# Kernel tuning notes

Measured on AMD Instinct MI355X. Metric: run time of the kernel, lower is better.

The kernel has to match this reference:

```python
import jax, jax.numpy as jnp
import numpy as np

N_NODES = 100000
N_EDGES = 1600000
IN_DIM, HID_DIM, OUT_DIM = 256, 128, 128


def gcn_norm(edge_index, edge_weight, num_nodes):
    # Add self-loops with weight 1 (PyG GCNConv default fill_value=1.0)
    loop = jnp.arange(num_nodes, dtype=edge_index.dtype)
    src = jnp.concatenate([edge_index[0], loop])
    dst = jnp.concatenate([edge_index[1], loop])
    w = jnp.concatenate([edge_weight, jnp.ones((num_nodes,), edge_weight.dtype)])
    # Symmetric normalization: deg computed at destination over edge weights
    deg = jax.ops.segment_sum(w, dst, num_segments=num_nodes)
    dinv = jnp.where(deg > 0, jax.lax.rsqrt(deg), 0.0)
    norm = dinv[src] * w * dinv[dst]  # [E + N]
    return src, dst, norm


def gcn_conv(x, W, b, src, dst, norm, num_nodes):
    h = x @ W                                  # [N, out]
    msg = h[src] * norm[:, None]               # gather + scale, [E+N, out]
    out = jax.ops.segment_sum(msg, dst, num_segments=num_nodes)  # scatter-add
    return out + b


def setup_inputs() -> dict:
    key = jax.random.key(0)
    ks = jax.random.split(key, 8)
    x = jax.random.normal(ks[0], (N_NODES, IN_DIM), dtype=jnp.float32)
    edge_index = jax.random.randint(ks[1], (2, N_EDGES), 0, N_NODES, dtype=jnp.int64)
    edge_weight = jax.random.uniform(ks[2], (N_EDGES,), dtype=jnp.float32)
    s1 = 1.0 / np.sqrt(IN_DIM)
    s2 = 1.0 / np.sqrt(HID_DIM)
    W1 = jax.random.uniform(ks[3], (IN_DIM, HID_DIM), jnp.float32, -s1, s1)
    b1 = jnp.zeros((HID_DIM,), jnp.float32)
    W2 = jax.random.uniform(ks[4], (HID_DIM, OUT_DIM), jnp.float32, -s2, s2)
    b2 = jnp.zeros((OUT_DIM,), jnp.float32)
    return {"x": x, "edge_index": edge_index, "edge_weight": edge_weight,
            "W1": W1, "b1": b1, "W2": W2, "b2": b2}


def reference(x, edge_index, edge_weight, W1, b1, W2, b2):
    n = x.shape[0]
    src, dst, norm = gcn_norm(edge_index, edge_weight, n)
    h = jax.nn.relu(gcn_conv(x, W1, b1, src, dst, norm, n))
    out = gcn_conv(h, W2, b2, src, dst, norm, n)
    return out
```

## Files before the change

### kernel.cpp

```cpp
#include <hip/hip_runtime.h>
#include <stdint.h>

#define N_NODES 100000
#define N_EDGES 1600000
#define IN_DIM 256
#define HID_DIM 128
#define OUT_DIM 128

#define NBUCK 391
#define CHUNK 4096
#define BCAP 4736

typedef __attribute__((ext_vector_type(8))) short short8;
typedef __attribute__((ext_vector_type(4))) float floatx4;

__device__ __forceinline__ float bf2f(unsigned short u) {
    union { unsigned int i; float f; } v; v.i = ((unsigned int)u) << 16; return v.f;
}
__device__ __forceinline__ unsigned short f2bf(float f) {
    union { float fl; unsigned int i; } v; v.fl = f;
    unsigned int x = v.i;
    return (unsigned short)((x + 0x7fffu + ((x >> 16) & 1u)) >> 16);
}
__device__ __forceinline__ float bflo(unsigned int u) {
    union { unsigned int i; float f; } v; v.i = u << 16; return v.f;
}
__device__ __forceinline__ float bfhi(unsigned int u) {
    union { unsigned int i; float f; } v; v.i = u & 0xffff0000u; return v.f;
}
__device__ __forceinline__ float asf(unsigned int u) {
    union { unsigned int i; float f; } v; v.i = u; return v.f;
}
__device__ __forceinline__ unsigned int asu(float f) {
    union { float fl; unsigned int i; } v; v.fl = f; return v.i;
}
__device__ __forceinline__ unsigned int pack2(float a, float b) {
    unsigned int ua = asu(a), ub = asu(b);
    ua += 0x7fffu + ((ua >> 16) & 1u);
    ub += 0x7fffu + ((ub >> 16) & 1u);
    return (ua >> 16) | (ub & 0xffff0000u);
}
__device__ __forceinline__ short8 pack8(float4 a, float4 b) {
    union { unsigned int u[4]; short8 s; } r;
    r.u[0] = pack2(a.x, a.y);
    r.u[1] = pack2(a.z, a.w);
    r.u[2] = pack2(b.x, b.y);
    r.u[3] = pack2(b.z, b.w);
    return r.s;
}

__global__ void k_detect(const unsigned int* __restrict__ xu, const unsigned int* __restrict__ eu,
                         int* __restrict__ flags, int* __restrict__ bucket_cursor) {
    __shared__ int s_huge, s_odd;
    if (threadIdx.x == 0) { s_huge = 0; s_odd = 0; }
    if (threadIdx.x < NBUCK) bucket_cursor[threadIdx.x] = 0;
    __syncthreads();
    int huge = 0, odd = 0;
    for (int i = threadIdx.x; i < 1024; i += 512) {
        unsigned int b = xu[i];
        unsigned int e = (b >> 23) & 0xffu;
        if (e >= 0xf0u) huge = 1;
        if (eu[2 * i + 1] != 0) odd = 1;
    }
    if (huge) atomicOr(&s_huge, 1);
    if (odd) atomicOr(&s_odd, 1);
    __syncthreads();
    if (threadIdx.x == 0) { flags[0] = s_huge ? 0 : 1; flags[1] = s_odd ? 0 : 1; }
}

__device__ __forceinline__ int load_idx(const void* base, long long i, int i64m) {
    int v = i64m ? (int)((const long long*)base)[i] : ((const int*)base)[i];
    return v < 0 ? 0 : (v >= N_NODES ? N_NODES - 1 : v);
}
__device__ __forceinline__ float load_f(const void* base, long long i, int f32m) {
    return f32m ? ((const float*)base)[i] : bf2f(((const unsigned short*)base)[i]);
}

__global__ void k_bscatter(const void* __restrict__ ei, const void* __restrict__ ew,
                           const int* __restrict__ flags, int* __restrict__ bucket_cursor,
                           uint2* __restrict__ ebuf, int e) {
    __shared__ int h[NBUCK];
    for (int t = threadIdx.x; t < NBUCK; t += 256) h[t] = 0;
    __syncthreads();
    int f32m = flags[0], i64m = flags[1];
    int base = blockIdx.x * CHUNK;
    int end = base + CHUNK < e ? base + CHUNK : e;
    for (int i = base + threadIdx.x; i < end; i += 256) {
        int d = load_idx(ei, (long long)N_EDGES + i, i64m);
        atomicAdd(&h[d >> 8], 1);
    }
    __syncthreads();
    for (int t = threadIdx.x; t < NBUCK; t += 256) {
        int c = h[t];
        h[t] = c ? (t * BCAP + atomicAdd(&bucket_cursor[t], c)) : 0;
    }
    __syncthreads();
    for (int i = base + threadIdx.x; i < end; i += 256) {
        int s = load_idx(ei, i, i64m);
        int d = load_idx(ei, (long long)N_EDGES + i, i64m);
        float w = load_f(ew, i, f32m);
        int b = d >> 8;
        int p = atomicAdd(&h[b], 1);
        uint2 c; c.x = (unsigned int)s | ((unsigned int)(d & 255) << 17); c.y = asu(w);
        ebuf[p] = c;
    }
}

__global__ void k_bscan(const int* __restrict__ bucket_cursor, int* __restrict__ bucket_base,
                        int* __restrict__ rowptr) {
    __shared__ int lds[512];
    int t = threadIdx.x;
    int v = (t < NBUCK) ? bucket_cursor[t] : 0;
    lds[t] = v;
    __syncthreads();
    for (int off = 1; off < 512; off <<= 1) {
        int x = (t >= off) ? lds[t - off] : 0;
        __syncthreads();
        lds[t] += x;
        __syncthreads();
    }
    int excl = lds[t] - v;
    if (t < NBUCK) bucket_base[t] = excl;
    if (t == 0) { bucket_base[NBUCK] = lds[NBUCK - 1]; rowptr[N_NODES] = N_EDGES; }
}

__global__ void k_fine(const uint2* __restrict__ ebuf, const int* __restrict__ bucket_base,
                       uint2* __restrict__ csr, int* __restrict__ rowptr,
                       float* __restrict__ dinv, int n) {
    __shared__ int h[256];
    __shared__ float fw[256];
    __shared__ int c2[256];
    int t = threadIdx.x, b = blockIdx.x;
    int w0 = bucket_base[b];
    int cnt = bucket_base[b + 1] - w0;
    const uint2* src = ebuf + (size_t)b * BCAP;
    if (t < 256) { h[t] = 0; fw[t] = 0.f; }
    __syncthreads();
    for (int i = t; i < cnt; i += 512) {
        uint2 c = src[i];
        int dl = (c.x >> 17) & 255;
        atomicAdd(&h[dl], 1);
        atomicAdd(&fw[dl], asf(c.y));
    }
    __syncthreads();
    int own = (t < 256) ? h[t] : 0;
    for (int off = 1; off < 256; off <<= 1) {
        int x = (t >= off && t < 256) ? h[t - off] : 0;
        __syncthreads();
        if (t < 256) h[t] += x;
        __syncthreads();
    }
    if (t < 256) {
        int excl = h[t] - own;
        int node = (b << 8) + t;
        if (node < n) {
            rowptr[node] = w0 + excl;
            dinv[node] = rsqrtf(1.0f + fw[t]);
        }
        c2[t] = w0 + excl;
    }
    __syncthreads();
    for (int i = t; i < cnt; i += 512) {
        uint2 c = src[i];
        int dl = (c.x >> 17) & 255;
        int p = atomicAdd(&c2[dl], 1);
        csr[p] = c;
    }
}

__global__ void k_transpose(const void* __restrict__ W1, const void* __restrict__ W2,
                            const int* __restrict__ flags,
                            unsigned short* __restrict__ W1T, unsigned short* __restrict__ W2T) {
    int i = blockIdx.x * 256 + threadIdx.x;
    int f32m = flags[0];
    if (i < IN_DIM * HID_DIM) {
        int k = i / HID_DIM, n = i % HID_DIM;
        W1T[n * IN_DIM + k] = f2bf(load_f(W1, i, f32m));
    } else {
        int j = i - IN_DIM * HID_DIM;
        if (j < HID_DIM * OUT_DIM) {
            int k = j / OUT_DIM, n = j % OUT_DIM;
            W2T[n * HID_DIM + k] = f2bf(load_f(W2, j, f32m));
        }
    }
}

template <int KH, bool F32M>
__device__ __forceinline__ void gemm_loop(const void* __restrict__ A,
                                          const unsigned short* __restrict__ Bs,
                                          size_t aoff, int quad, int l16, floatx4 (&acc)[8]) {
    constexpr int NCH = KH / 32;
    constexpr int BMASK = KH / 8 - 1;
    short8 a[NCH];
    if (F32M) {
        const float* ap = (const float*)A;
#pragma unroll
        for (int ch = 0; ch < NCH; ch++) {
            float4 f0 = *(const float4*)(ap + aoff + ch * 32);
            float4 f1 = *(const float4*)(ap + aoff + ch * 32 + 4);
            a[ch] = pack8(f0, f1);
        }
    } else {
        const unsigned short* ap = (const unsigned short*)A;
#pragma unroll
        for (int ch = 0; ch < NCH; ch++)
            a[ch] = *(const short8*)(ap + aoff + ch * 32);
    }
#pragma unroll
    for (int ch = 0; ch < NCH; ch++) {
#pragma unroll
        for (int c = 0; c < 8; c++) {
            int col = c * 16 + l16;
            int boff = col * KH + 8 * ((ch * 4 + quad + (col & 7)) & BMASK);
            short8 bf = *(const short8*)(Bs + boff);
            acc[c] = __builtin_amdgcn_mfma_f32_16x16x32_bf16(a[ch], bf, acc[c], 0, 0, 0);
        }
    }
}

template <int K, bool RAWA>
__global__ void k_gemm(const void* __restrict__ A, const unsigned short* __restrict__ WT,
                       const float* __restrict__ dinv, unsigned short* __restrict__ H,
                       const int* __restrict__ flags, int n) {
    constexpr int KH = 64;
    __shared__ unsigned short Bs[128 * KH];

    int wave = threadIdx.x >> 6;
    int lane = threadIdx.x & 63;
    int quad = lane >> 4;
    int l16 = lane & 15;
    int rowbase = blockIdx.x * 64 + wave * 16;
    int r0 = rowbase + l16;        if (r0 >= n) r0 = n - 1;
    size_t aoff0 = (size_t)r0 * K + quad * 8;

    floatx4 acc[8];
#pragma unroll
    for (int c = 0; c < 8; c++) acc[c] = (floatx4){0.f, 0.f, 0.f, 0.f};

    int f32m = RAWA ? flags[0] : 0;

#pragma unroll
    for (int hh = 0; hh < K / KH; hh++) {
        if (hh) __syncthreads();
        for (int base = threadIdx.x * 8; base < 128 * KH; base += 256 * 8) {
            int col = base / KH;
            int k = base - col * KH;
            int ks = (k + (col & 7) * 8) & (KH - 1);
            *(short8*)(&Bs[col * KH + ks]) = *(const short8*)(WT + col * K + hh * KH + k);
        }
        __syncthreads();
        if (RAWA && f32m)
            gemm_loop<KH, true>(A, Bs, aoff0 + hh * KH, quad, l16, acc);
        else
            gemm_loop<KH, false>(A, Bs, aoff0 + hh * KH, quad, l16, acc);
    }

#pragma unroll
    for (int r = 0; r < 4; r++) {
        int grow = rowbase + quad * 4 + r;
        if (grow < n) {
            float sc = dinv[grow];
#pragma unroll
            for (int c = 0; c < 8; c++)
                H[(size_t)grow * 128 + c * 16 + l16] = f2bf(sc * acc[c][r]);
        }
    }
}

#define NODES_PER_BLK 16

__device__ __forceinline__ void acc8(float wt, uint4 hv, float* a) {
    a[0] += wt * bflo(hv.x); a[1] += wt * bfhi(hv.x);
    a[2] += wt * bflo(hv.y); a[3] += wt * bfhi(hv.y);
    a[4] += wt * bflo(hv.z); a[5] += wt * bfhi(hv.z);
    a[6] += wt * bflo(hv.w); a[7] += wt * bfhi(hv.w);
}

template <bool RELU, bool FINAL>
__global__ void k_aggregate(const unsigned short* __restrict__ H, const int* __restrict__ rowptr,
                            const uint2* __restrict__ csr, const float* __restrict__ dinv,
                            const void* __restrict__ bias, void* __restrict__ out,
                            const int* __restrict__ flags, int n) {
    __shared__ int cursor;
    if (threadIdx.x == 0) cursor = 0;
    __syncthreads();
    int lane = threadIdx.x & 15;
    int col = lane * 8;
    int f32m = flags[0];

    float bv[8];
#pragma unroll
    for (int i = 0; i < 8; i++) bv[i] = load_f(bias, col + i, f32m);

    for (;;) {
        int idx;
        if (lane == 0) idx = atomicAdd(&cursor, 1);
        idx = __shfl(idx, 0, 16);
        if (idx >= NODES_PER_BLK) break;
        int node = blockIdx.x * NODES_PER_BLK + idx;
        if (node >= n) break;

        int e0 = rowptr[node], e1 = rowptr[node + 1];
        uint4 u = *(const uint4*)(H + (size_t)node * 128 + col);
        float dn = dinv[node];

        float a[8] = {0.f, 0.f, 0.f, 0.f, 0.f, 0.f, 0.f, 0.f};
        int e = e0;
        for (; e + 4 <= e1; e += 4) {
            uint2 c0 = csr[e], c1 = csr[e + 1], c2 = csr[e + 2], c3 = csr[e + 3];
            uint4 h0 = *(const uint4*)(H + (size_t)(c0.x & 0x1FFFF) * 128 + col);
            uint4 h1 = *(const uint4*)(H + (size_t)(c1.x & 0x1FFFF) * 128 + col);
            uint4 h2 = *(const uint4*)(H + (size_t)(c2.x & 0x1FFFF) * 128 + col);
            uint4 h3 = *(const uint4*)(H + (size_t)(c3.x & 0x1FFFF) * 128 + col);
            acc8(asf(c0.y), h0, a); acc8(asf(c1.y), h1, a);
            acc8(asf(c2.y), h2, a); acc8(asf(c3.y), h3, a);
        }
        for (; e < e1; e++) {
            uint2 c = csr[e];
            uint4 hh = *(const uint4*)(H + (size_t)(c.x & 0x1FFFF) * 128 + col);
            acc8(asf(c.y), hh, a);
        }

        a[0] = dn * (a[0] + bflo(u.x)) + bv[0];
        a[1] = dn * (a[1] + bfhi(u.x)) + bv[1];
        a[2] = dn * (a[2] + bflo(u.y)) + bv[2];
        a[3] = dn * (a[3] + bfhi(u.y)) + bv[3];
        a[4] = dn * (a[4] + bflo(u.z)) + bv[4];
        a[5] = dn * (a[5] + bfhi(u.z)) + bv[5];
        a[6] = dn * (a[6] + bflo(u.w)) + bv[6];
        a[7] = dn * (a[7] + bfhi(u.w)) + bv[7];

        if (RELU) {
#pragma unroll
            for (int i = 0; i < 8; i++) a[i] = fmaxf(a[i], 0.f);
        }
        if (FINAL && f32m) {
            float* op = (float*)out + (size_t)node * 128 + col;
            float4 o0 = {a[0], a[1], a[2], a[3]};
            float4 o1 = {a[4], a[5], a[6], a[7]};
            *(float4*)op = o0;
            *(float4*)(op + 4) = o1;
        } else {
            uint4 o;
            o.x = pack2(a[0], a[1]); o.y = pack2(a[2], a[3]);
            o.z = pack2(a[4], a[5]); o.w = pack2(a[6], a[7]);
            *(uint4*)((unsigned short*)out + (size_t)node * 128 + col) = o;
        }
    }
}

extern "C" void kernel_launch(void* const* d_in, const int* in_sizes, int n_in,
                              void* d_out, int out_size, void* d_ws, size_t ws_size,
                              hipStream_t stream) {
    const void* x  = d_in[0];
    const void* ei = d_in[1];
    const void* ew = d_in[2];
    const void* W1 = d_in[3];
    const void* b1 = d_in[4];
    const void* W2 = d_in[5];
    const void* b2 = d_in[6];

    char* p = (char*)d_ws;
    auto alloc = [&](size_t bytes) { char* r = p; p += (bytes + 255) & ~(size_t)255; return r; };
    int*   flags    = (int*)alloc(256);
    float* dinv     = (float*)alloc((size_t)N_NODES * 4);
    int*   rowptr   = (int*)alloc((size_t)(N_NODES + 1) * 4);
    int*   bucket_cursor = (int*)alloc((size_t)NBUCK * 4);
    int*   bucket_base   = (int*)alloc((size_t)(NBUCK + 1) * 4);
    uint2* csr      = (uint2*)alloc((size_t)N_EDGES * 8);
    unsigned short* W1T  = (unsigned short*)alloc((size_t)IN_DIM * HID_DIM * 2);
    unsigned short* W2T  = (unsigned short*)alloc((size_t)HID_DIM * OUT_DIM * 2);
    unsigned short* hbuf = (unsigned short*)alloc((size_t)N_NODES * 128 * 2);
    unsigned short* zbuf = (unsigned short*)alloc((size_t)N_NODES * 128 * 2);
    uint2* ebuf = (uint2*)hbuf;

    int nbC = (N_EDGES + CHUNK - 1) / CHUNK;
    int nbG = (N_NODES + 63) / 64;
    int nbA = (N_NODES + NODES_PER_BLK - 1) / NODES_PER_BLK;

    k_detect<<<1, 512, 0, stream>>>((const unsigned int*)x, (const unsigned int*)ei, flags, bucket_cursor);
    k_bscatter<<<nbC, 256, 0, stream>>>(ei, ew, flags, bucket_cursor, ebuf, N_EDGES);
    k_bscan<<<1, 512, 0, stream>>>(bucket_cursor, bucket_base, rowptr);
    k_fine<<<NBUCK, 512, 0, stream>>>(ebuf, bucket_base, csr, rowptr, dinv, N_NODES);
    k_transpose<<<(IN_DIM * HID_DIM + HID_DIM * OUT_DIM + 255) / 256, 256, 0, stream>>>(W1, W2, flags, W1T, W2T);

    k_gemm<IN_DIM, true><<<nbG, 256, 0, stream>>>(x, W1T, dinv, hbuf, flags, N_NODES);
    k_aggregate<true, false><<<nbA, 256, 0, stream>>>(hbuf, rowptr, csr, dinv,
                                                      b1, zbuf, flags, N_NODES);
    k_gemm<HID_DIM, false><<<nbG, 256, 0, stream>>>(zbuf, W2T, dinv, hbuf, flags, N_NODES);
    k_aggregate<false, true><<<nbA, 256, 0, stream>>>(hbuf, rowptr, csr, dinv,
                                                      b2, d_out, flags, N_NODES);
}
```

Measured before the change: 413.3 us.

## Stage full weight matrix in LDS and issue all A loads before sync

Result: no change. 412.7 us (-0.1%).

```diff
diff --git a/kernel.cpp b/kernel.cpp
--- a/kernel.cpp
+++ b/kernel.cpp
@@ -185,74 +185,63 @@
     }
 }
 
-template <int KH, bool F32M>
-__device__ __forceinline__ void gemm_loop(const void* __restrict__ A,
-                                          const unsigned short* __restrict__ Bs,
-                                          size_t aoff, int quad, int l16, floatx4 (&acc)[8]) {
-    constexpr int NCH = KH / 32;
-    constexpr int BMASK = KH / 8 - 1;
-    short8 a[NCH];
-    if (F32M) {
-        const float* ap = (const float*)A;
-#pragma unroll
-        for (int ch = 0; ch < NCH; ch++) {
-            float4 f0 = *(const float4*)(ap + aoff + ch * 32);
-            float4 f1 = *(const float4*)(ap + aoff + ch * 32 + 4);
-            a[ch] = pack8(f0, f1);
-        }
-    } else {
-        const unsigned short* ap = (const unsigned short*)A;
-#pragma unroll
-        for (int ch = 0; ch < NCH; ch++)
-            a[ch] = *(const short8*)(ap + aoff + ch * 32);
-    }
-#pragma unroll
-    for (int ch = 0; ch < NCH; ch++) {
-#pragma unroll
-        for (int c = 0; c < 8; c++) {
-            int col = c * 16 + l16;
-            int boff = col * KH + 8 * ((ch * 4 + quad + (col & 7)) & BMASK);
-            short8 bf = *(const short8*)(Bs + boff);
-            acc[c] = __builtin_amdgcn_mfma_f32_16x16x32_bf16(a[ch], bf, acc[c], 0, 0, 0);
-        }
-    }
-}
-
 template <int K, bool RAWA>
 __global__ void k_gemm(const void* __restrict__ A, const unsigned short* __restrict__ WT,
                        const float* __restrict__ dinv, unsigned short* __restrict__ H,
                        const int* __restrict__ flags, int n) {
-    constexpr int KH = 64;
-    __shared__ unsigned short Bs[128 * KH];
+    __shared__ unsigned short Bs[128 * K];
+    constexpr int NCH = K / 32;
+    constexpr int BMASK = K / 8 - 1;
 
     int wave = threadIdx.x >> 6;
     int lane = threadIdx.x & 63;
     int quad = lane >> 4;
     int l16 = lane & 15;
-    int rowbase = blockIdx.x * 64 + wave * 16;
+    int rowbase = blockIdx.x * 128 + wave * 16;
     int r0 = rowbase + l16;        if (r0 >= n) r0 = n - 1;
-    size_t aoff0 = (size_t)r0 * K + quad * 8;
+    size_t aoff = (size_t)r0 * K + quad * 8;
+
+    for (int base = threadIdx.x * 8; base < 128 * K; base += 512 * 8) {
+        int col = base / K;
+        int k = base - col * K;
+        int ks = (k + (col & 7) * 8) & (K - 1);
+        *(short8*)(&Bs[col * K + ks]) = *(const short8*)(WT + base);
+    }
+
+    short8 a[NCH];
+    int f32m = RAWA ? flags[0] : 0;
+    if (RAWA && f32m) {
+        const float* ap = (const float*)A;
+        float4 f[NCH][2];
+#pragma unroll
+        for (int ch = 0; ch < NCH; ch++) {
+            f[ch][0] = *(const float4*)(ap + aoff + ch * 32);
+            f[ch][1] = *(const float4*)(ap + aoff + ch * 32 + 4);
+        }
+#pragma unroll
+        for (int ch = 0; ch < NCH; ch++) a[ch] = pack8(f[ch][0], f[ch][1]);
+    } else {
+        const unsigned short* ap = (const unsigned short*)A;
+#pragma unroll
+        for (int ch = 0; ch < NCH; ch++)
+            a[ch] = *(const short8*)(ap + aoff + ch * 32);
+    }
+
+    __syncthreads();
 
     floatx4 acc[8];
 #pragma unroll
     for (int c = 0; c < 8; c++) acc[c] = (floatx4){0.f, 0.f, 0.f, 0.f};
 
-    int f32m = RAWA ? flags[0] : 0;
-
-#pragma unroll
-    for (int hh = 0; hh < K / KH; hh++) {
-        if (hh) __syncthreads();
-        for (int base = threadIdx.x * 8; base < 128 * KH; base += 256 * 8) {
-            int col = base / KH;
-            int k = base - col * KH;
-            int ks = (k + (col & 7) * 8) & (KH - 1);
-            *(short8*)(&Bs[col * KH + ks]) = *(const short8*)(WT + col * K + hh * KH + k);
-        }
-        __syncthreads();
-        if (RAWA && f32m)
-            gemm_loop<KH, true>(A, Bs, aoff0 + hh * KH, quad, l16, acc);
-        else
-            gemm_loop<KH, false>(A, Bs, aoff0 + hh * KH, quad, l16, acc);
+#pragma unroll
+    for (int ch = 0; ch < NCH; ch++) {
+#pragma unroll
+        for (int c = 0; c < 8; c++) {
+            int col = c * 16 + l16;
+            int boff = col * K + 8 * ((ch * 4 + quad + (col & 7)) & BMASK);
+            short8 bf = *(const short8*)(Bs + boff);
+            acc[c] = __builtin_amdgcn_mfma_f32_16x16x32_bf16(a[ch], bf, acc[c], 0, 0, 0);
+        }
     }
 
 #pragma unroll
@@ -375,7 +364,7 @@
     uint2* ebuf = (uint2*)hbuf;
 
     int nbC = (N_EDGES + CHUNK - 1) / CHUNK;
-    int nbG = (N_NODES + 63) / 64;
+    int nbG = (N_NODES + 127) / 128;
     int nbA = (N_NODES + NODES_PER_BLK - 1) / NODES_PER_BLK;
 
     k_detect<<<1, 512, 0, stream>>>((const unsigned int*)x, (const unsigned int*)ei, flags, bucket_cursor);
@@ -384,10 +373,10 @@
     k_fine<<<NBUCK, 512, 0, stream>>>(ebuf, bucket_base, csr, rowptr, dinv, N_NODES);
     k_transpose<<<(IN_DIM * HID_DIM + HID_DIM * OUT_DIM + 255) / 256, 256, 0, stream>>>(W1, W2, flags, W1T, W2T);
 
-    k_gemm<IN_DIM, true><<<nbG, 256, 0, stream>>>(x, W1T, dinv, hbuf, flags, N_NODES);
+    k_gemm<IN_DIM, true><<<nbG, 512, 0, stream>>>(x, W1T, dinv, hbuf, flags, N_NODES);
     k_aggregate<true, false><<<nbA, 256, 0, stream>>>(hbuf, rowptr, csr, dinv,
                                                       b1, zbuf, flags, N_NODES);
-    k_gemm<HID_DIM, false><<<nbG, 256, 0, stream>>>(zbuf, W2T, dinv, hbuf, flags, N_NODES);
+    k_gemm<HID_DIM, false><<<nbG, 512, 0, stream>>>(zbuf, W2T, dinv, hbuf, flags, N_NODES);
     k_aggregate<false, true><<<nbA, 256, 0, stream>>>(hbuf, rowptr, csr, dinv,
                                                       b2, d_out, flags, N_NODES);
 }
```
